# Performance work log

Hardware: AMD Instinct MI355X
Metric: run time of the kernel (lower is better)

The kernel has to match this reference:

```python
import jax, jax.numpy as jnp
import numpy as np

NUM_LAYERS = 2
D_MODEL = 64
D_INNER = 128   # expand * d_model
D_STATE = 128   # min(2*input_size, 256)
DT_RANK = 4     # ceil(d_model / 16)
D_CONV = 4
HIDDEN = 64


def _causal_dwconv(x, w, b):
    # x: [B, L, C], w: [C, K], b: [C]  -- causal depthwise conv (left pad K-1)
    K = w.shape[1]
    L = x.shape[1]
    xp = jnp.pad(x, ((0, 0), (K - 1, 0), (0, 0)))
    y = sum(xp[:, k:k + L, :] * w[:, k][None, None, :] for k in range(K))
    return y + b


def _selective_scan(u, delta, A, B, C, Dp):
    # u, delta: [b,L,d]; A: [d,n]; B, C: [b,L,n]; Dp: [d]
    dA = jnp.exp(jnp.einsum('bld,dn->lbdn', delta, A))          # [L,b,d,n]
    dBu = jnp.einsum('bld,bln,bld->lbdn', delta, B, u)           # [L,b,d,n]
    Ct = jnp.swapaxes(C, 0, 1)                                   # [L,b,n]

    def step(h, inp):
        dA_t, dBu_t, C_t = inp
        h = dA_t * h + dBu_t                                     # [b,d,n]
        y = jnp.einsum('bdn,bn->bd', h, C_t)
        return h, y

    h0 = jnp.zeros(dA.shape[1:], dA.dtype)
    _, ys = jax.lax.scan(step, h0, (dA, dBu, Ct))                # ys: [L,b,d]
    return jnp.swapaxes(ys, 0, 1) + u * Dp


def _mamba_layer(x, in_w, conv_w, conv_b, xproj_w, dt_w, dt_b, A_log, Dp, out_w):
    xz = x @ in_w.T                                              # [B,L,2*d_inner]
    xi, z = jnp.split(xz, 2, axis=-1)
    xi = jax.nn.silu(_causal_dwconv(xi, conv_w, conv_b))
    xdbl = xi @ xproj_w.T                                        # [B,L,dt_rank+2*d_state]
    delta = jax.nn.softplus(xdbl[..., :DT_RANK] @ dt_w.T + dt_b)
    Bm = xdbl[..., DT_RANK:DT_RANK + D_STATE]
    Cm = xdbl[..., DT_RANK + D_STATE:]
    A = -jnp.exp(A_log)
    y = _selective_scan(xi, delta, A, Bm, Cm, Dp)
    y = y * jax.nn.silu(z)
    return y @ out_w.T


def setup_inputs() -> dict:
    key = jax.random.key(0)
    ks = jax.random.split(key, 10)
    B, L = 4, 1024
    s = 0.05
    x = jax.random.normal(ks[0], (B, L, D_MODEL), dtype=jnp.float32)
    in_proj_w = jax.random.normal(ks[1], (NUM_LAYERS, 2 * D_INNER, D_MODEL)) * s
    conv_w = jax.random.normal(ks[2], (NUM_LAYERS, D_INNER, D_CONV)) * 0.2
    conv_b = jax.random.normal(ks[3], (NUM_LAYERS, D_INNER)) * 0.02
    x_proj_w = jax.random.normal(ks[4], (NUM_LAYERS, DT_RANK + 2 * D_STATE, D_INNER)) * s
    dt_w = jax.random.normal(ks[5], (NUM_LAYERS, D_INNER, DT_RANK)) * 0.1
    dt_b = jnp.full((NUM_LAYERS, D_INNER), -4.6, dtype=jnp.float32)  # softplus -> ~0.01
    # S4D-real init: A_log = log(1..d_state)
    A_log = jnp.log(jnp.broadcast_to(
        jnp.arange(1, D_STATE + 1, dtype=jnp.float32), (NUM_LAYERS, D_INNER, D_STATE)))
    D = jnp.ones((NUM_LAYERS, D_INNER), dtype=jnp.float32)
    out_proj_w = jax.random.normal(ks[6], (NUM_LAYERS, D_MODEL, D_INNER)) * s
    fc_w = jax.random.normal(ks[7], (HIDDEN, D_MODEL)) * s
    fc_b = jax.random.normal(ks[8], (HIDDEN,)) * 0.02
    return {"x": x, "in_proj_w": in_proj_w, "conv_w": conv_w, "conv_b": conv_b,
            "x_proj_w": x_proj_w, "dt_w": dt_w, "dt_b": dt_b, "A_log": A_log,
            "D": D, "out_proj_w": out_proj_w, "fc_w": fc_w, "fc_b": fc_b}


def reference(x, in_proj_w, conv_w, conv_b, x_proj_w, dt_w, dt_b, A_log, D, out_proj_w, fc_w, fc_b):
    h = x
    for l in range(NUM_LAYERS):
        h = _mamba_layer(h, in_proj_w[l], conv_w[l], conv_b[l], x_proj_w[l],
                         dt_w[l], dt_b[l], A_log[l], D[l], out_proj_w[l])
    return h @ fc_w.T + fc_b
```

## Files before the change

### kernel.cpp

```cpp
#include <hip/hip_runtime.h>
#include <hip/hip_bf16.h>

#define BB 4
#define LL 1024
#define DM 64
#define DI 128
#define DS 128
#define DTR 4
#define KC 4
#define RT 8
#define GRP 8
#define CS 64
#define NC 16
#define SCD 8
#define QL 32
#define L2E 1.44269504f

#define XWT_OFF   0
#define INWT_OFF  65536
#define OWT_OFF   98304
#define CWT_OFF   114688
#define CB_OFF    115712
#define DTWT_OFF  115968
#define DTB_OFF   116992
#define XWDT_OFF  117248

__device__ __forceinline__ float silu_f(float x) { return x / (1.f + __expf(-x)); }
__device__ __forceinline__ float ex2(float x) { return __builtin_amdgcn_exp2f(x); }

__device__ __forceinline__ float ldf(const void* p, long i, unsigned bf) {
    return bf ? __bfloat162float(((const __hip_bfloat16*)p)[i]) : ((const float*)p)[i];
}

__device__ __forceinline__ void fma4(float4& acc, float s, const float4 w) {
    acc.x = fmaf(s, w.x, acc.x); acc.y = fmaf(s, w.y, acc.y);
    acc.z = fmaf(s, w.z, acc.z); acc.w = fmaf(s, w.w, acc.w);
}

__device__ __forceinline__ void probe_flags(const void* dtb, const void* fcw,
                                            unsigned& bfe, unsigned& bfw) {
    unsigned w = *(const unsigned*)dtb;
    bfe = (w == 0xC093C093u) ? 1u : 0u;
    const unsigned* p = (const unsigned*)fcw;
    int cnt = 0;
    for (int i = 0; i < 32; ++i) {
        unsigned m = p[i] & 0x7FFFu;
        if (m >= 0x3000u && m < 0x4200u) cnt++;
    }
    bfw = (cnt >= 28) ? 1u : 0u;
}

__global__ __launch_bounds__(256) void k_prep(
        const void* __restrict__ inw, const void* __restrict__ xw,
        const void* __restrict__ ow, const void* __restrict__ cw,
        const void* __restrict__ cb, const void* __restrict__ dtw,
        const void* __restrict__ dtb, const void* __restrict__ fcw,
        unsigned* __restrict__ flags, float* __restrict__ WT) {
    unsigned bfe, bfw;
    probe_flags(dtb, fcw, bfe, bfw);
    int bid = blockIdx.x, tid = threadIdx.x;
    if (bid < 28) {
        const void* src; long soff; int srcK; float* dst; int dstN; int n0, k0;
        if (bid < 16) {
            int l = bid >> 3, kt = (bid >> 2) & 1, nt = bid & 3;
            src = xw; srcK = 128; soff = (long)l * 260 * 128 + 4 * 128;
            n0 = nt * 64; k0 = kt * 64; dst = WT + XWT_OFF + l * 32768; dstN = 256;
        } else if (bid < 24) {
            int b2 = bid - 16, l = b2 >> 2, nt = b2 & 3;
            src = inw; srcK = 64; soff = (long)l * 256 * 64;
            n0 = nt * 64; k0 = 0; dst = WT + INWT_OFF + l * 16384; dstN = 256;
        } else {
            int b2 = bid - 24, l = b2 >> 1, kt = b2 & 1;
            src = ow; srcK = 128; soff = (long)l * 64 * 128;
            n0 = 0; k0 = kt * 64; dst = WT + OWT_OFF + l * 8192; dstN = 64;
        }
        __shared__ float tile[64 * 65];
        for (int i = tid; i < 4096; i += 256) {
            int ln = i >> 6, lk = i & 63;
            tile[ln * 65 + lk] = ldf(src, soff + (long)(n0 + ln) * srcK + k0 + lk, bfw);
        }
        __syncthreads();
        for (int i = tid; i < 4096; i += 256) {
            int lk = i >> 6, ln = i & 63;
            dst[(long)(k0 + lk) * dstN + n0 + ln] = tile[ln * 65 + lk];
        }
    } else {
        if (tid == 0) { flags[0] = bfe; flags[1] = bfw; flags[2] = bfe & bfw; }
        for (int j = tid; j < 1024; j += 256) {
            int l = j >> 9, t = (j >> 7) & 3, d = j & 127;
            WT[CWT_OFF + j] = ldf(cw, (long)l * 512 + d * 4 + t, bfw);
        }
        for (int j = tid; j < 256; j += 256) WT[CB_OFF + j] = ldf(cb, j, bfw);
        for (int j = tid; j < 1024; j += 256) {
            int l = j >> 9, r = (j >> 7) & 3, d = j & 127;
            WT[DTWT_OFF + j] = ldf(dtw, (long)l * 512 + d * 4 + r, bfw);
        }
        for (int j = tid; j < 256; j += 256) WT[DTB_OFF + j] = ldf(dtb, j, bfe);
        for (int j = tid; j < 1024; j += 256) {
            int l = j >> 9, rem = j & 511;
            WT[XWDT_OFF + j] = ldf(xw, (long)l * 260 * 128 + rem, bfw);
        }
    }
}

__global__ __launch_bounds__(256) void k_inproj(
        const void* __restrict__ xin, int xin_probe,
        const float* __restrict__ wt, const unsigned* __restrict__ flags,
        float* __restrict__ xzx, float* __restrict__ sz) {
    unsigned bfx = xin_probe ? flags[0] : 0u;
    int row0 = blockIdx.x * RT;
    int tid = threadIdx.x, lane = tid & 63, g = tid >> 6;
    __shared__ float act[RT * DM];
    for (int i = tid; i < RT * DM; i += 256)
        act[i] = ldf(xin, (long)(row0 + (i >> 6)) * DM + (i & 63), bfx);
    __syncthreads();
    const float4* wt4 = (const float4*)wt;
    float4 acc[2];
    acc[0] = make_float4(0.f, 0.f, 0.f, 0.f);
    acc[1] = make_float4(0.f, 0.f, 0.f, 0.f);
#pragma unroll 8
    for (int k4 = 0; k4 < DM / 4; ++k4) {
        float4 w0 = wt4[(k4 * 4 + 0) * 64 + lane];
        float4 w1 = wt4[(k4 * 4 + 1) * 64 + lane];
        float4 w2 = wt4[(k4 * 4 + 2) * 64 + lane];
        float4 w3 = wt4[(k4 * 4 + 3) * 64 + lane];
#pragma unroll
        for (int r = 0; r < 2; ++r) {
            float4 av = *(const float4*)&act[(g * 2 + r) * DM + k4 * 4];
            fma4(acc[r], av.x, w0); fma4(acc[r], av.y, w1);
            fma4(acc[r], av.z, w2); fma4(acc[r], av.w, w3);
        }
    }
    int n0 = lane * 4;
#pragma unroll
    for (int r = 0; r < 2; ++r) {
        int row = row0 + g * 2 + r;
        if (n0 < DI) {
            *(float4*)&xzx[(size_t)row * DI + n0] = acc[r];
        } else {
            float4 v;
            v.x = silu_f(acc[r].x); v.y = silu_f(acc[r].y);
            v.z = silu_f(acc[r].z); v.w = silu_f(acc[r].w);
            *(float4*)&sz[(size_t)row * DI + (n0 - DI)] = v;
        }
    }
}

__global__ __launch_bounds__(256) void k_xproj(
        const float* __restrict__ xzx,
        const float* __restrict__ cwT, const float* __restrict__ cbF,
        const float* __restrict__ xwT, const float* __restrict__ xwdtF,
        const float* __restrict__ dtwT, const float* __restrict__ dtbF,
        float* __restrict__ xiw, float* __restrict__ dlt,
        float* __restrict__ Bm, float* __restrict__ Cm) {
    int row0 = blockIdx.x * RT;
    int b = row0 >> 10, l0 = row0 & (LL - 1);
    int tid = threadIdx.x, lane = tid & 63, g = tid >> 6;
    __shared__ float xc[(RT + KC - 1) * DI];
    __shared__ float act[RT * DI];
    __shared__ float dtp[RT * DTR];
    for (int i = tid; i < (RT + KC - 1) * DI; i += 256) {
        int r = (i >> 7) - (KC - 1);
        int l = l0 + r;
        xc[i] = (l >= 0) ? xzx[((size_t)b * LL + l) * DI + (i & 127)] : 0.f;
    }
    __syncthreads();
    for (int i = tid; i < RT * DI; i += 256) {
        int r = i >> 7, d = i & 127;
        float a = cbF[d];
#pragma unroll
        for (int t = 0; t < KC; ++t) a = fmaf(xc[(r + t) * DI + d], cwT[t * DI + d], a);
        float v = silu_f(a);
        act[i] = v;
        xiw[(size_t)(row0 + r) * DI + d] = v;
    }
    __syncthreads();
    const float4* wt4 = (const float4*)xwT;
    float4 acc[2];
    acc[0] = make_float4(0.f, 0.f, 0.f, 0.f);
    acc[1] = make_float4(0.f, 0.f, 0.f, 0.f);
#pragma unroll 8
    for (int k4 = 0; k4 < DI / 4; ++k4) {
        float4 w0 = wt4[(k4 * 4 + 0) * 64 + lane];
        float4 w1 = wt4[(k4 * 4 + 1) * 64 + lane];
        float4 w2 = wt4[(k4 * 4 + 2) * 64 + lane];
        float4 w3 = wt4[(k4 * 4 + 3) * 64 + lane];
#pragma unroll
        for (int r = 0; r < 2; ++r) {
            float4 av = *(const float4*)&act[(g * 2 + r) * DI + k4 * 4];
            fma4(acc[r], av.x, w0); fma4(acc[r], av.y, w1);
            fma4(acc[r], av.z, w2); fma4(acc[r], av.w, w3);
        }
    }
    int n0 = lane * 4;
#pragma unroll
    for (int r = 0; r < 2; ++r) {
        int row = row0 + g * 2 + r;
        if (n0 < DS) *(float4*)&Bm[(size_t)row * DS + n0] = acc[r];
        else         *(float4*)&Cm[(size_t)row * DS + (n0 - DS)] = acc[r];
    }
    if (tid < RT * DTR) {
        int r = tid >> 2, i = tid & 3;
        float a = 0.f;
#pragma unroll
        for (int k4 = 0; k4 < DI / 4; ++k4) {
            float4 av = *(const float4*)&act[r * DI + k4 * 4];
            float4 wv = *(const float4*)&xwdtF[i * DI + k4 * 4];
            a = fmaf(av.x, wv.x, a); a = fmaf(av.y, wv.y, a);
            a = fmaf(av.z, wv.z, a); a = fmaf(av.w, wv.w, a);
        }
        dtp[tid] = a;
    }
    __syncthreads();
    if (tid < DI) {
        float dw0 = dtwT[0 * DI + tid], dw1 = dtwT[1 * DI + tid];
        float dw2 = dtwT[2 * DI + tid], dw3 = dtwT[3 * DI + tid];
        float bv = dtbF[tid];
#pragma unroll
        for (int r = 0; r < RT; ++r) {
            float a = bv;
            a = fmaf(dtp[r * 4 + 0], dw0, a);
            a = fmaf(dtp[r * 4 + 1], dw1, a);
            a = fmaf(dtp[r * 4 + 2], dw2, a);
            a = fmaf(dtp[r * 4 + 3], dw3, a);
            dlt[(size_t)(row0 + r) * DI + tid] = (a > 20.f) ? a : log1pf(__expf(a));
        }
    }
}

__global__ __launch_bounds__(512) void k_scan1(
        const float* __restrict__ dlt, const float* __restrict__ xiw,
        const float* __restrict__ Bm, const float* __restrict__ Cm,
        const void* __restrict__ Alog, long aoff,
        const void* __restrict__ Dp, long doff,
        const unsigned* __restrict__ flags,
        float* __restrict__ hend, float* __restrict__ S,
        float* __restrict__ y) {
    __shared__ float Bsh[QL][DS];
    __shared__ float Csh[QL][DS];
    __shared__ float dsh[SCD][CS];
    __shared__ float dush[SCD][CS];
    __shared__ float ysh[CS][SCD];
    __shared__ float Wred[SCD * 520];
    int gid = blockIdx.x;
    int dg = gid / (BB * NC);
    int bc = gid % (BB * NC);
    int b = bc / NC, c = bc % NC;
    int d0 = dg * SCD;
    int tid = threadIdx.x, w = tid >> 6, t = tid & 63;
    int d = d0 + w, c0 = c * CS;
    unsigned bfe = flags[0];
    float A0 = -L2E * __expf(ldf(Alog, aoff + (long)d * DS + 2 * t, bfe));
    float A1 = -L2E * __expf(ldf(Alog, aoff + (long)d * DS + 2 * t + 1, bfe));
    {
        size_t src = ((size_t)b * LL + c0 + t) * DI + d0 + w;
        float dl = dlt[src], ul = xiw[src];
        dsh[w][t] = dl;
        dush[w][t] = dl * ul;
        ysh[t][w] = ul * ldf(Dp, doff + d0 + w, bfe);
    }
    float* Wl = Wred + w * 520;
    int rbase = (t >> 3) * 65 + (t & 7) * 8;
    float h0 = 0.f, h1v = 0.f, sumd = 0.f;
    for (int hh = 0; hh < 2; ++hh) {
        __syncthreads();
        for (int i = tid; i < QL * 32; i += 512) {
            int r = i >> 5, c4 = (i & 31) * 4;
            size_t g = ((size_t)b * LL + c0 + hh * QL + r) * DS + c4;
            *(float4*)&Bsh[r][c4] = *(const float4*)&Bm[g];
            *(float4*)&Csh[r][c4] = *(const float4*)&Cm[g];
        }
        __syncthreads();
        for (int li = 0; li < QL; li += GRP) {
            int lg = hh * QL + li;
            float dl[GRP], du[GRP], ea0[GRP], ea1[GRP], cv[GRP];
            float2 Bv[GRP], Cv[GRP];
#pragma unroll
            for (int s = 0; s < GRP; ++s) {
                dl[s] = dsh[w][lg + s];
                du[s] = dush[w][lg + s];
                Bv[s] = ((const float2*)Bsh[li + s])[t];
                Cv[s] = ((const float2*)Csh[li + s])[t];
            }
#pragma unroll
            for (int s = 0; s < GRP; ++s) {
                ea0[s] = ex2(dl[s] * A0);
                ea1[s] = ex2(dl[s] * A1);
                sumd += dl[s];
            }
#pragma unroll
            for (int s = 0; s < GRP; ++s) {
                h0  = fmaf(ea0[s], h0,  du[s] * Bv[s].x);
                h1v = fmaf(ea1[s], h1v, du[s] * Bv[s].y);
                cv[s] = fmaf(h0, Cv[s].x, h1v * Cv[s].y);
            }
#pragma unroll
            for (int s = 0; s < GRP; ++s) Wl[s * 65 + t] = cv[s];
            float pt = 0.f;
#pragma unroll
            for (int j = 0; j < 8; ++j) pt += Wl[rbase + j];
            pt += __shfl_xor(pt, 1, 64);
            pt += __shfl_xor(pt, 2, 64);
            pt += __shfl_xor(pt, 4, 64);
            if ((t & 7) == 0) ysh[lg + (t >> 3)][w] += pt;
        }
    }
    if (c < NC - 1) {
        size_t hbase = (((size_t)b * DI + d) * NC + c) * DS;
        ((float2*)(hend + hbase))[t] = make_float2(h0, h1v);
        if (t == 0) S[((size_t)b * DI + d) * NC + c] = sumd;
    }
    __syncthreads();
    for (int i = tid; i < CS * SCD; i += 512) {
        int l = i >> 3, dd = i & 7;
        y[((size_t)b * LL + c0 + l) * DI + d0 + dd] = ysh[l][dd];
    }
}

__global__ __launch_bounds__(512) void k_scan2(
        const float* __restrict__ dlt, const float* __restrict__ Cm,
        const void* __restrict__ Alog, long aoff,
        const unsigned* __restrict__ flags,
        const float* __restrict__ hend, const float* __restrict__ S,
        float* __restrict__ y) {
    __shared__ float Csh[QL][DS];
    __shared__ float cdsh[SCD][CS];
    __shared__ float ysh[CS][SCD];
    __shared__ float Wred[SCD * 520];
    int gid = blockIdx.x;
    int dg = gid / (BB * (NC - 1));
    int bc = gid % (BB * (NC - 1));
    int b = bc / (NC - 1), c = bc % (NC - 1) + 1;
    int d0 = dg * SCD;
    int tid = threadIdx.x, w = tid >> 6, t = tid & 63;
    int d = d0 + w, c0 = c * CS;
    unsigned bfe = flags[0];
    float A0 = -L2E * __expf(ldf(Alog, aoff + (long)d * DS + 2 * t, bfe));
    float A1 = -L2E * __expf(ldf(Alog, aoff + (long)d * DS + 2 * t + 1, bfe));
    {
        float a = dlt[((size_t)b * LL + c0 + t) * DI + d0 + w];
#pragma unroll
        for (int off = 1; off < 64; off <<= 1) {
            float nn = __shfl(a, t - off, 64);
            if (t >= off) a += nn;
        }
        cdsh[w][t] = a;
    }
    float hi0 = 0.f, hi1 = 0.f, ssum = 0.f;
    const float2* hep = (const float2*)(hend + (((size_t)b * DI + d) * NC) * DS);
    const float* Sp = S + ((size_t)b * DI + d) * NC;
    for (int cc = c - 1; cc >= 0; --cc) {
        float2 he = hep[(size_t)cc * (DS / 2) + t];
        hi0 = fmaf(ex2(A0 * ssum), he.x, hi0);
        hi1 = fmaf(ex2(A1 * ssum), he.y, hi1);
        ssum += Sp[cc];
    }
    float* Wl = Wred + w * 520;
    int rbase = (t >> 3) * 65 + (t & 7) * 8;
    for (int hh = 0; hh < 2; ++hh) {
        __syncthreads();
        for (int i = tid; i < QL * 32; i += 512) {
            int r = i >> 5, c4 = (i & 31) * 4;
            *(float4*)&Csh[r][c4] =
                *(const float4*)&Cm[((size_t)b * LL + c0 + hh * QL + r) * DS + c4];
        }
        __syncthreads();
        for (int li = 0; li < QL; li += GRP) {
            int lg = hh * QL + li;
            float cd[GRP], ea0[GRP], ea1[GRP], cv[GRP];
            float2 Cv[GRP];
#pragma unroll
            for (int s = 0; s < GRP; ++s) {
                cd[s] = cdsh[w][lg + s];
                Cv[s] = ((const float2*)Csh[li + s])[t];
            }
#pragma unroll
            for (int s = 0; s < GRP; ++s) {
                ea0[s] = ex2(cd[s] * A0);
                ea1[s] = ex2(cd[s] * A1);
            }
#pragma unroll
            for (int s = 0; s < GRP; ++s)
                cv[s] = fmaf(hi0 * ea0[s], Cv[s].x, hi1 * ea1[s] * Cv[s].y);
#pragma unroll
            for (int s = 0; s < GRP; ++s) Wl[s * 65 + t] = cv[s];
            float pt = 0.f;
#pragma unroll
            for (int j = 0; j < 8; ++j) pt += Wl[rbase + j];
            pt += __shfl_xor(pt, 1, 64);
            pt += __shfl_xor(pt, 2, 64);
            pt += __shfl_xor(pt, 4, 64);
            if ((t & 7) == 0) ysh[lg + (t >> 3)][w] = pt;
        }
    }
    __syncthreads();
    for (int i = tid; i < CS * SCD; i += 512) {
        int l = i >> 3, dd = i & 7;
        size_t idx = ((size_t)b * LL + c0 + l) * DI + d0 + dd;
        y[idx] += ysh[l][dd];
    }
}

__global__ __launch_bounds__(256) void k_out(
        const float* __restrict__ y, const float* __restrict__ sz,
        const float* __restrict__ owT, float* __restrict__ hout) {
    int row0 = blockIdx.x * RT;
    int tid = threadIdx.x, n = tid & 63, g = tid >> 6;
    __shared__ float act[RT * DI];
    for (int i = tid; i < RT * DI; i += 256) {
        size_t idx = (size_t)(row0 + (i >> 7)) * DI + (i & 127);
        act[i] = y[idx] * sz[idx];
    }
    __syncthreads();
    float acc[2] = {0.f, 0.f};
#pragma unroll 8
    for (int k4 = 0; k4 < DI / 4; ++k4) {
        float w0 = owT[(k4 * 4 + 0) * DM + n];
        float w1 = owT[(k4 * 4 + 1) * DM + n];
        float w2 = owT[(k4 * 4 + 2) * DM + n];
        float w3 = owT[(k4 * 4 + 3) * DM + n];
#pragma unroll
        for (int r = 0; r < 2; ++r) {
            float4 av = *(const float4*)&act[(g * 2 + r) * DI + k4 * 4];
            acc[r] = fmaf(av.x, w0, acc[r]); acc[r] = fmaf(av.y, w1, acc[r]);
            acc[r] = fmaf(av.z, w2, acc[r]); acc[r] = fmaf(av.w, w3, acc[r]);
        }
    }
#pragma unroll
    for (int r = 0; r < 2; ++r)
        hout[(size_t)(row0 + g * 2 + r) * DM + n] = acc[r];
}

__global__ __launch_bounds__(256) void k_fc(
        const float* __restrict__ h, const void* __restrict__ fw,
        const void* __restrict__ fb, const unsigned* __restrict__ flags,
        void* __restrict__ out) {
    unsigned bfw = flags[1], obf = flags[2];
    int row0 = blockIdx.x * RT;
    int tid = threadIdx.x, n = tid & 63, g = tid >> 6;
    __shared__ float wsh[DM * 65];
    __shared__ float act[RT * DM];
    for (int i = tid; i < DM * DM; i += 256) {
        int nn = i >> 6, k = i & 63;
        wsh[k * 65 + nn] = ldf(fw, i, bfw);
    }
    for (int i = tid; i < RT * DM; i += 256)
        act[i] = h[(size_t)(row0 + (i >> 6)) * DM + (i & 63)];
    __syncthreads();
    float bv = ldf(fb, n, bfw);
    float acc[2] = {bv, bv};
#pragma unroll 8
    for (int k4 = 0; k4 < DM / 4; ++k4) {
        float w0 = wsh[(k4 * 4 + 0) * 65 + n];
        float w1 = wsh[(k4 * 4 + 1) * 65 + n];
        float w2 = wsh[(k4 * 4 + 2) * 65 + n];
        float w3 = wsh[(k4 * 4 + 3) * 65 + n];
#pragma unroll
        for (int r = 0; r < 2; ++r) {
            float4 av = *(const float4*)&act[(g * 2 + r) * DM + k4 * 4];
            acc[r] = fmaf(av.x, w0, acc[r]); acc[r] = fmaf(av.y, w1, acc[r]);
            acc[r] = fmaf(av.z, w2, acc[r]); acc[r] = fmaf(av.w, w3, acc[r]);
        }
    }
#pragma unroll
    for (int r = 0; r < 2; ++r) {
        size_t idx = (size_t)(row0 + g * 2 + r) * DM + n;
        if (obf) ((__hip_bfloat16*)out)[idx] = __float2bfloat16(acc[r]);
        else     ((float*)out)[idx] = acc[r];
    }
}

extern "C" void kernel_launch(void* const* d_in, const int* in_sizes, int n_in,
                              void* d_out, int out_size, void* d_ws, size_t ws_size,
                              hipStream_t stream) {
    const void* x    = d_in[0];
    const void* inw  = d_in[1];
    const void* cw   = d_in[2];
    const void* cb   = d_in[3];
    const void* xw   = d_in[4];
    const void* dtw  = d_in[5];
    const void* dtb  = d_in[6];
    const void* Alog = d_in[7];
    const void* Dp   = d_in[8];
    const void* ow   = d_in[9];
    const void* fcw  = d_in[10];
    const void* fcb  = d_in[11];

    const size_t NBL = (size_t)BB * LL;
    const int GB = (int)(NBL / RT);
    unsigned* flags = (unsigned*)d_ws;
    float* base = (float*)d_ws + 64;
    float* h1   = base;
    float* sz   = h1 + 262144;
    float* xiw  = sz + 524288;
    float* dlt  = xiw + 524288;
    float* Bmw  = dlt + 524288;
    float* Cmw  = Bmw + 524288;
    float* yw   = Cmw + 524288;
    float* hend = yw + 524288;
    float* S    = hend + 1048576;
    float* xzx  = yw;
    float* WT   = (float*)d_out;

    k_prep<<<29, 256, 0, stream>>>(inw, xw, ow, cw, cb, dtw, dtb, fcw, flags, WT);

    for (int l = 0; l < 2; ++l) {
        const void* xin = (l == 0) ? x : (const void*)h1;
        int xmode = (l == 0) ? 1 : 0;
        k_inproj<<<GB, 256, 0, stream>>>(xin, xmode, WT + INWT_OFF + l * 16384, flags, xzx, sz);
        k_xproj<<<GB, 256, 0, stream>>>(xzx,
                                        WT + CWT_OFF + l * 512, WT + CB_OFF + l * 128,
                                        WT + XWT_OFF + l * 32768, WT + XWDT_OFF + l * 512,
                                        WT + DTWT_OFF + l * 512, WT + DTB_OFF + l * 128,
                                        xiw, dlt, Bmw, Cmw);
        long ao = (long)l * DI * DS;
        long dof = (long)l * DI;
        k_scan1<<<(DI / SCD) * BB * NC, 512, 0, stream>>>(
            dlt, xiw, Bmw, Cmw, Alog, ao, Dp, dof, flags, hend, S, yw);
        k_scan2<<<(DI / SCD) * BB * (NC - 1), 512, 0, stream>>>(
            dlt, Cmw, Alog, ao, flags, hend, S, yw);
        k_out<<<GB, 256, 0, stream>>>(yw, sz, WT + OWT_OFF + l * 8192, h1);
    }
    k_fc<<<GB, 256, 0, stream>>>(h1, fcw, fcb, flags, d_out);
}
```

Measured before the change: 292.1 us.

## Fuse all layer stages into one cooperative persistent kernel with grid syncs

Replaces the per-layer chain of eleven kernel launches with a single cooperative kernel. It loops over tiles for each stage and separates stages with grid-wide syncs, and the scan work is re-tiled to 4 channels per 256-thread block. The aim is to remove launch overhead and inter-kernel gaps. In exchange it adds the cost of grid barriers and threadfences, caps the grid at nb*256 blocks with nb at most 8, and the smaller scan tiles change how loads are reused.

Result: slower. 979.8 us (+235.4%).

```diff
diff --git a/kernel.cpp b/kernel.cpp
--- a/kernel.cpp
+++ b/kernel.cpp
@@ -1,5 +1,8 @@
 #include <hip/hip_runtime.h>
 #include <hip/hip_bf16.h>
+#include <hip/hip_cooperative_groups.h>
+
+namespace cg = cooperative_groups;
 
 #define BB 4
 #define LL 1024
@@ -12,8 +15,8 @@
 #define GRP 8
 #define CS 64
 #define NC 16
-#define SCD 8
-#define QL 32
+#define SCD 4
+#define QL 16
 #define L2E 1.44269504f
 
 #define XWT_OFF   0
@@ -103,6 +106,390 @@
     }
 }
 
+
+struct SM_s1 {
+    float Bsh[QL][DS];
+    float Csh[QL][DS];
+    float dsh[SCD][CS];
+    float dush[SCD][CS];
+    float ysh[CS][SCD];
+    float Wred[SCD * 520];
+};
+struct SM_s2 {
+    float Csh[QL][DS];
+    float cdsh[SCD][CS];
+    float ysh[CS][SCD];
+    float Wred[SCD * 520];
+};
+struct SM_ip { float act[RT * DM]; };
+struct SM_xp { float xc[(RT + KC - 1) * DI]; float act[RT * DI]; float dtp[RT * DTR]; };
+struct SM_o  { float act[RT * DI]; };
+struct SM_f  { float wsh[DM * 65]; float act[RT * DM]; };
+union SMem {
+    SM_s1 s1; SM_s2 s2; SM_ip ip; SM_xp xp; SM_o o; SM_f f;
+};
+
+__global__ __launch_bounds__(256) void k_mega(
+        const void* __restrict__ x, const float* __restrict__ WT,
+        const unsigned* __restrict__ flags,
+        float* __restrict__ h1, float* __restrict__ sz,
+        float* __restrict__ xiw, float* __restrict__ dlt,
+        float* __restrict__ Bm, float* __restrict__ Cm,
+        float* __restrict__ y, float* __restrict__ hend, float* __restrict__ S,
+        const void* __restrict__ Alog, const void* __restrict__ Dp,
+        const void* __restrict__ fcw, const void* __restrict__ fcb,
+        void* __restrict__ out) {
+    cg::grid_group grid = cg::this_grid();
+    __shared__ SMem sm;
+    int tid = threadIdx.x;
+    int lane = tid & 63, g4 = tid >> 6;
+    unsigned bfe = flags[0], bfw = flags[1], obf = flags[2];
+    float* xzx = y;
+
+    for (int l = 0; l < 2; ++l) {
+        const float* inwT  = WT + INWT_OFF + l * 16384;
+        const float* xwT   = WT + XWT_OFF + l * 32768;
+        const float* cwT   = WT + CWT_OFF + l * 512;
+        const float* cbF   = WT + CB_OFF + l * 128;
+        const float* dtwT  = WT + DTWT_OFF + l * 512;
+        const float* dtbF  = WT + DTB_OFF + l * 128;
+        const float* xwdtF = WT + XWDT_OFF + l * 512;
+        const float* owT   = WT + OWT_OFF + l * 8192;
+        long aoff = (long)l * DI * DS;
+        long doff = (long)l * DI;
+        const void* xin = (l == 0) ? x : (const void*)h1;
+        unsigned bfx = (l == 0) ? bfe : 0u;
+
+        for (int tile = blockIdx.x; tile < 512; tile += gridDim.x) {
+            __syncthreads();
+            int row0 = tile * RT;
+            for (int i = tid; i < RT * DM; i += 256)
+                sm.ip.act[i] = ldf(xin, (long)(row0 + (i >> 6)) * DM + (i & 63), bfx);
+            __syncthreads();
+            const float4* wt4 = (const float4*)inwT;
+            float4 acc[2];
+            acc[0] = make_float4(0.f, 0.f, 0.f, 0.f);
+            acc[1] = make_float4(0.f, 0.f, 0.f, 0.f);
+#pragma unroll 8
+            for (int k4 = 0; k4 < DM / 4; ++k4) {
+                float4 w0 = wt4[(k4 * 4 + 0) * 64 + lane];
+                float4 w1 = wt4[(k4 * 4 + 1) * 64 + lane];
+                float4 w2 = wt4[(k4 * 4 + 2) * 64 + lane];
+                float4 w3 = wt4[(k4 * 4 + 3) * 64 + lane];
+#pragma unroll
+                for (int r = 0; r < 2; ++r) {
+                    float4 av = *(const float4*)&sm.ip.act[(g4 * 2 + r) * DM + k4 * 4];
+                    fma4(acc[r], av.x, w0); fma4(acc[r], av.y, w1);
+                    fma4(acc[r], av.z, w2); fma4(acc[r], av.w, w3);
+                }
+            }
+            int n0 = lane * 4;
+#pragma unroll
+            for (int r = 0; r < 2; ++r) {
+                int row = row0 + g4 * 2 + r;
+                if (n0 < DI) {
+                    *(float4*)&xzx[(size_t)row * DI + n0] = acc[r];
+                } else {
+                    float4 v;
+                    v.x = silu_f(acc[r].x); v.y = silu_f(acc[r].y);
+                    v.z = silu_f(acc[r].z); v.w = silu_f(acc[r].w);
+                    *(float4*)&sz[(size_t)row * DI + (n0 - DI)] = v;
+                }
+            }
+        }
+        __threadfence(); grid.sync();
+
+        for (int tile = blockIdx.x; tile < 512; tile += gridDim.x) {
+            __syncthreads();
+            int row0 = tile * RT;
+            int b = row0 >> 10, l0 = row0 & (LL - 1);
+            for (int i = tid; i < (RT + KC - 1) * DI; i += 256) {
+                int r = (i >> 7) - (KC - 1);
+                int ll2 = l0 + r;
+                sm.xp.xc[i] = (ll2 >= 0) ? xzx[((size_t)b * LL + ll2) * DI + (i & 127)] : 0.f;
+            }
+            __syncthreads();
+            for (int i = tid; i < RT * DI; i += 256) {
+                int r = i >> 7, d = i & 127;
+                float a = cbF[d];
+#pragma unroll
+                for (int t = 0; t < KC; ++t)
+                    a = fmaf(sm.xp.xc[(r + t) * DI + d], cwT[t * DI + d], a);
+                float v = silu_f(a);
+                sm.xp.act[i] = v;
+                xiw[(size_t)(row0 + r) * DI + d] = v;
+            }
+            __syncthreads();
+            const float4* wt4 = (const float4*)xwT;
+            float4 acc[2];
+            acc[0] = make_float4(0.f, 0.f, 0.f, 0.f);
+            acc[1] = make_float4(0.f, 0.f, 0.f, 0.f);
+#pragma unroll 8
+            for (int k4 = 0; k4 < DI / 4; ++k4) {
+                float4 w0 = wt4[(k4 * 4 + 0) * 64 + lane];
+                float4 w1 = wt4[(k4 * 4 + 1) * 64 + lane];
+                float4 w2 = wt4[(k4 * 4 + 2) * 64 + lane];
+                float4 w3 = wt4[(k4 * 4 + 3) * 64 + lane];
+#pragma unroll
+                for (int r = 0; r < 2; ++r) {
+                    float4 av = *(const float4*)&sm.xp.act[(g4 * 2 + r) * DI + k4 * 4];
+                    fma4(acc[r], av.x, w0); fma4(acc[r], av.y, w1);
+                    fma4(acc[r], av.z, w2); fma4(acc[r], av.w, w3);
+                }
+            }
+            int n0 = lane * 4;
+#pragma unroll
+            for (int r = 0; r < 2; ++r) {
+                int row = row0 + g4 * 2 + r;
+                if (n0 < DS) *(float4*)&Bm[(size_t)row * DS + n0] = acc[r];
+                else         *(float4*)&Cm[(size_t)row * DS + (n0 - DS)] = acc[r];
+            }
+            if (tid < RT * DTR) {
+                int r = tid >> 2, i = tid & 3;
+                float a = 0.f;
+#pragma unroll
+                for (int k4 = 0; k4 < DI / 4; ++k4) {
+                    float4 av = *(const float4*)&sm.xp.act[r * DI + k4 * 4];
+                    float4 wv = *(const float4*)&xwdtF[i * DI + k4 * 4];
+                    a = fmaf(av.x, wv.x, a); a = fmaf(av.y, wv.y, a);
+                    a = fmaf(av.z, wv.z, a); a = fmaf(av.w, wv.w, a);
+                }
+                sm.xp.dtp[tid] = a;
+            }
+            __syncthreads();
+            if (tid < DI) {
+                float dw0 = dtwT[0 * DI + tid], dw1 = dtwT[1 * DI + tid];
+                float dw2 = dtwT[2 * DI + tid], dw3 = dtwT[3 * DI + tid];
+                float bv = dtbF[tid];
+#pragma unroll
+                for (int r = 0; r < RT; ++r) {
+                    float a = bv;
+                    a = fmaf(sm.xp.dtp[r * 4 + 0], dw0, a);
+                    a = fmaf(sm.xp.dtp[r * 4 + 1], dw1, a);
+                    a = fmaf(sm.xp.dtp[r * 4 + 2], dw2, a);
+                    a = fmaf(sm.xp.dtp[r * 4 + 3], dw3, a);
+                    dlt[(size_t)(row0 + r) * DI + tid] = (a > 20.f) ? a : log1pf(__expf(a));
+                }
+            }
+        }
+        __threadfence(); grid.sync();
+
+        for (int u = blockIdx.x; u < (DI / SCD) * BB * NC; u += gridDim.x) {
+            __syncthreads();
+            int dg = u >> 6;
+            int bc = u & 63;
+            int b = bc >> 4, c = bc & 15;
+            int d0 = dg * SCD;
+            int w = g4, t = lane;
+            int d = d0 + w, c0 = c * CS;
+            float A0 = -L2E * __expf(ldf(Alog, aoff + (long)d * DS + 2 * t, bfe));
+            float A1 = -L2E * __expf(ldf(Alog, aoff + (long)d * DS + 2 * t + 1, bfe));
+            {
+                size_t src = ((size_t)b * LL + c0 + t) * DI + d0 + w;
+                float dl = dlt[src], ul = xiw[src];
+                sm.s1.dsh[w][t] = dl;
+                sm.s1.dush[w][t] = dl * ul;
+                sm.s1.ysh[t][w] = ul * ldf(Dp, doff + d0 + w, bfe);
+            }
+            float* Wl = sm.s1.Wred + w * 520;
+            int rbase = (t >> 3) * 65 + (t & 7) * 8;
+            float h0 = 0.f, h1v = 0.f, sumd = 0.f;
+            for (int qq = 0; qq < CS / QL; ++qq) {
+                __syncthreads();
+                for (int i = tid; i < QL * 32; i += 256) {
+                    int r = i >> 5, c4 = (i & 31) * 4;
+                    size_t gsrc = ((size_t)b * LL + c0 + qq * QL + r) * DS + c4;
+                    *(float4*)&sm.s1.Bsh[r][c4] = *(const float4*)&Bm[gsrc];
+                    *(float4*)&sm.s1.Csh[r][c4] = *(const float4*)&Cm[gsrc];
+                }
+                __syncthreads();
+                for (int li = 0; li < QL; li += GRP) {
+                    int lg = qq * QL + li;
+                    float dl[GRP], du[GRP], ea0[GRP], ea1[GRP], cv[GRP];
+                    float2 Bv[GRP], Cv[GRP];
+#pragma unroll
+                    for (int s = 0; s < GRP; ++s) {
+                        dl[s] = sm.s1.dsh[w][lg + s];
+                        du[s] = sm.s1.dush[w][lg + s];
+                        Bv[s] = ((const float2*)sm.s1.Bsh[li + s])[t];
+                        Cv[s] = ((const float2*)sm.s1.Csh[li + s])[t];
+                    }
+#pragma unroll
+                    for (int s = 0; s < GRP; ++s) {
+                        ea0[s] = ex2(dl[s] * A0);
+                        ea1[s] = ex2(dl[s] * A1);
+                        sumd += dl[s];
+                    }
+#pragma unroll
+                    for (int s = 0; s < GRP; ++s) {
+                        h0  = fmaf(ea0[s], h0,  du[s] * Bv[s].x);
+                        h1v = fmaf(ea1[s], h1v, du[s] * Bv[s].y);
+                        cv[s] = fmaf(h0, Cv[s].x, h1v * Cv[s].y);
+                    }
+#pragma unroll
+                    for (int s = 0; s < GRP; ++s) Wl[s * 65 + t] = cv[s];
+                    float pt = 0.f;
+#pragma unroll
+                    for (int j = 0; j < 8; ++j) pt += Wl[rbase + j];
+                    pt += __shfl_xor(pt, 1, 64);
+                    pt += __shfl_xor(pt, 2, 64);
+                    pt += __shfl_xor(pt, 4, 64);
+                    if ((t & 7) == 0) sm.s1.ysh[lg + (t >> 3)][w] += pt;
+                }
+            }
+            if (c < NC - 1) {
+                size_t hbase = (((size_t)b * DI + d) * NC + c) * DS;
+                ((float2*)(hend + hbase))[t] = make_float2(h0, h1v);
+                if (t == 0) S[((size_t)b * DI + d) * NC + c] = sumd;
+            }
+            __syncthreads();
+            for (int i = tid; i < CS * SCD; i += 256) {
+                int ll2 = i >> 2, dd = i & 3;
+                y[((size_t)b * LL + c0 + ll2) * DI + d0 + dd] = sm.s1.ysh[ll2][dd];
+            }
+        }
+        __threadfence(); grid.sync();
+
+        for (int u = blockIdx.x; u < (DI / SCD) * BB * (NC - 1); u += gridDim.x) {
+            __syncthreads();
+            int dg = u / (BB * (NC - 1));
+            int bc = u % (BB * (NC - 1));
+            int b = bc / (NC - 1), c = bc % (NC - 1) + 1;
+            int d0 = dg * SCD;
+            int w = g4, t = lane;
+            int d = d0 + w, c0 = c * CS;
+            float A0 = -L2E * __expf(ldf(Alog, aoff + (long)d * DS + 2 * t, bfe));
+            float A1 = -L2E * __expf(ldf(Alog, aoff + (long)d * DS + 2 * t + 1, bfe));
+            {
+                float a = dlt[((size_t)b * LL + c0 + t) * DI + d0 + w];
+#pragma unroll
+                for (int off = 1; off < 64; off <<= 1) {
+                    float nn = __shfl(a, t - off, 64);
+                    if (t >= off) a += nn;
+                }
+                sm.s2.cdsh[w][t] = a;
+            }
+            float hi0 = 0.f, hi1 = 0.f, ssum = 0.f;
+            const float2* hep = (const float2*)(hend + (((size_t)b * DI + d) * NC) * DS);
+            const float* Sp = S + ((size_t)b * DI + d) * NC;
+            for (int cc = c - 1; cc >= 0; --cc) {
+                float2 he = hep[(size_t)cc * (DS / 2) + t];
+                hi0 = fmaf(ex2(A0 * ssum), he.x, hi0);
+                hi1 = fmaf(ex2(A1 * ssum), he.y, hi1);
+                ssum += Sp[cc];
+            }
+            float* Wl = sm.s2.Wred + w * 520;
+            int rbase = (t >> 3) * 65 + (t & 7) * 8;
+            for (int qq = 0; qq < CS / QL; ++qq) {
+                __syncthreads();
+                for (int i = tid; i < QL * 32; i += 256) {
+                    int r = i >> 5, c4 = (i & 31) * 4;
+                    *(float4*)&sm.s2.Csh[r][c4] =
+                        *(const float4*)&Cm[((size_t)b * LL + c0 + qq * QL + r) * DS + c4];
+                }
+                __syncthreads();
+                for (int li = 0; li < QL; li += GRP) {
+                    int lg = qq * QL + li;
+                    float cd[GRP], ea0[GRP], ea1[GRP], cv[GRP];
+                    float2 Cv[GRP];
+#pragma unroll
+                    for (int s = 0; s < GRP; ++s) {
+                        cd[s] = sm.s2.cdsh[w][lg + s];
+                        Cv[s] = ((const float2*)sm.s2.Csh[li + s])[t];
+                    }
+#pragma unroll
+                    for (int s = 0; s < GRP; ++s) {
+                        ea0[s] = ex2(cd[s] * A0);
+                        ea1[s] = ex2(cd[s] * A1);
+                    }
+#pragma unroll
+                    for (int s = 0; s < GRP; ++s)
+                        cv[s] = fmaf(hi0 * ea0[s], Cv[s].x, hi1 * ea1[s] * Cv[s].y);
+#pragma unroll
+                    for (int s = 0; s < GRP; ++s) Wl[s * 65 + t] = cv[s];
+                    float pt = 0.f;
+#pragma unroll
+                    for (int j = 0; j < 8; ++j) pt += Wl[rbase + j];
+                    pt += __shfl_xor(pt, 1, 64);
+                    pt += __shfl_xor(pt, 2, 64);
+                    pt += __shfl_xor(pt, 4, 64);
+                    if ((t & 7) == 0) sm.s2.ysh[lg + (t >> 3)][w] = pt;
+                }
+            }
+            __syncthreads();
+            for (int i = tid; i < CS * SCD; i += 256) {
+                int ll2 = i >> 2, dd = i & 3;
+                size_t idx = ((size_t)b * LL + c0 + ll2) * DI + d0 + dd;
+                y[idx] += sm.s2.ysh[ll2][dd];
+            }
+        }
+        __threadfence(); grid.sync();
+
+        for (int tile = blockIdx.x; tile < 512; tile += gridDim.x) {
+            __syncthreads();
+            int row0 = tile * RT;
+            int n = lane;
+            for (int i = tid; i < RT * DI; i += 256) {
+                size_t idx = (size_t)(row0 + (i >> 7)) * DI + (i & 127);
+                sm.o.act[i] = y[idx] * sz[idx];
+            }
+            __syncthreads();
+            float acc[2] = {0.f, 0.f};
+#pragma unroll 8
+            for (int k4 = 0; k4 < DI / 4; ++k4) {
+                float w0 = owT[(k4 * 4 + 0) * DM + n];
+                float w1 = owT[(k4 * 4 + 1) * DM + n];
+                float w2 = owT[(k4 * 4 + 2) * DM + n];
+                float w3 = owT[(k4 * 4 + 3) * DM + n];
+#pragma unroll
+                for (int r = 0; r < 2; ++r) {
+                    float4 av = *(const float4*)&sm.o.act[(g4 * 2 + r) * DI + k4 * 4];
+                    acc[r] = fmaf(av.x, w0, acc[r]); acc[r] = fmaf(av.y, w1, acc[r]);
+                    acc[r] = fmaf(av.z, w2, acc[r]); acc[r] = fmaf(av.w, w3, acc[r]);
+                }
+            }
+#pragma unroll
+            for (int r = 0; r < 2; ++r)
+                h1[(size_t)(row0 + g4 * 2 + r) * DM + n] = acc[r];
+        }
+        __threadfence(); grid.sync();
+    }
+
+    for (int tile = blockIdx.x; tile < 512; tile += gridDim.x) {
+        __syncthreads();
+        int row0 = tile * RT;
+        int n = lane;
+        for (int i = tid; i < DM * DM; i += 256) {
+            int nn = i >> 6, k = i & 63;
+            sm.f.wsh[k * 65 + nn] = ldf(fcw, i, bfw);
+        }
+        for (int i = tid; i < RT * DM; i += 256)
+            sm.f.act[i] = h1[(size_t)(row0 + (i >> 6)) * DM + (i & 63)];
+        __syncthreads();
+        float bv = ldf(fcb, n, bfw);
+        float acc[2] = {bv, bv};
+#pragma unroll 8
+        for (int k4 = 0; k4 < DM / 4; ++k4) {
+            float w0 = sm.f.wsh[(k4 * 4 + 0) * 65 + n];
+            float w1 = sm.f.wsh[(k4 * 4 + 1) * 65 + n];
+            float w2 = sm.f.wsh[(k4 * 4 + 2) * 65 + n];
+            float w3 = sm.f.wsh[(k4 * 4 + 3) * 65 + n];
+#pragma unroll
+            for (int r = 0; r < 2; ++r) {
+                float4 av = *(const float4*)&sm.f.act[(g4 * 2 + r) * DM + k4 * 4];
+                acc[r] = fmaf(av.x, w0, acc[r]); acc[r] = fmaf(av.y, w1, acc[r]);
+                acc[r] = fmaf(av.z, w2, acc[r]); acc[r] = fmaf(av.w, w3, acc[r]);
+            }
+        }
+#pragma unroll
+        for (int r = 0; r < 2; ++r) {
+            size_t idx = (size_t)(row0 + g4 * 2 + r) * DM + n;
+            if (obf) ((__hip_bfloat16*)out)[idx] = __float2bfloat16(acc[r]);
+            else     ((float*)out)[idx] = acc[r];
+        }
+    }
+}
+
 __global__ __launch_bounds__(256) void k_inproj(
         const void* __restrict__ xin, int xin_probe,
         const float* __restrict__ wt, const unsigned* __restrict__ flags,
@@ -228,6 +615,7 @@
     }
 }
 
+#define FQL 32
 __global__ __launch_bounds__(512) void k_scan1(
         const float* __restrict__ dlt, const float* __restrict__ xiw,
         const float* __restrict__ Bm, const float* __restrict__ Cm,
@@ -236,17 +624,17 @@
         const unsigned* __restrict__ flags,
         float* __restrict__ hend, float* __restrict__ S,
         float* __restrict__ y) {
-    __shared__ float Bsh[QL][DS];
-    __shared__ float Csh[QL][DS];
-    __shared__ float dsh[SCD][CS];
-    __shared__ float dush[SCD][CS];
-    __shared__ float ysh[CS][SCD];
-    __shared__ float Wred[SCD * 520];
+    __shared__ float Bsh[FQL][DS];
+    __shared__ float Csh[FQL][DS];
+    __shared__ float dsh[8][CS];
+    __shared__ float dush[8][CS];
+    __shared__ float ysh[CS][8];
+    __shared__ float Wred[8 * 520];
     int gid = blockIdx.x;
     int dg = gid / (BB * NC);
     int bc = gid % (BB * NC);
     int b = bc / NC, c = bc % NC;
-    int d0 = dg * SCD;
+    int d0 = dg * 8;
     int tid = threadIdx.x, w = tid >> 6, t = tid & 63;
     int d = d0 + w, c0 = c * CS;
     unsigned bfe = flags[0];
@@ -264,15 +652,15 @@
     float h0 = 0.f, h1v = 0.f, sumd = 0.f;
     for (int hh = 0; hh < 2; ++hh) {
         __syncthreads();
-        for (int i = tid; i < QL * 32; i += 512) {
+        for (int i = tid; i < FQL * 32; i += 512) {
             int r = i >> 5, c4 = (i & 31) * 4;
-            size_t g = ((size_t)b * LL + c0 + hh * QL + r) * DS + c4;
+            size_t g = ((size_t)b * LL + c0 + hh * FQL + r) * DS + c4;
             *(float4*)&Bsh[r][c4] = *(const float4*)&Bm[g];
             *(float4*)&Csh[r][c4] = *(const float4*)&Cm[g];
         }
         __syncthreads();
-        for (int li = 0; li < QL; li += GRP) {
-            int lg = hh * QL + li;
+        for (int li = 0; li < FQL; li += GRP) {
+            int lg = hh * FQL + li;
             float dl[GRP], du[GRP], ea0[GRP], ea1[GRP], cv[GRP];
             float2 Bv[GRP], Cv[GRP];
 #pragma unroll
@@ -311,7 +699,7 @@
         if (t == 0) S[((size_t)b * DI + d) * NC + c] = sumd;
     }
     __syncthreads();
-    for (int i = tid; i < CS * SCD; i += 512) {
+    for (int i = tid; i < CS * 8; i += 512) {
         int l = i >> 3, dd = i & 7;
         y[((size_t)b * LL + c0 + l) * DI + d0 + dd] = ysh[l][dd];
     }
@@ -323,15 +711,15 @@
         const unsigned* __restrict__ flags,
         const float* __restrict__ hend, const float* __restrict__ S,
         float* __restrict__ y) {
-    __shared__ float Csh[QL][DS];
-    __shared__ float cdsh[SCD][CS];
-    __shared__ float ysh[CS][SCD];
-    __shared__ float Wred[SCD * 520];
+    __shared__ float Csh[FQL][DS];
+    __shared__ float cdsh[8][CS];
+    __shared__ float ysh[CS][8];
+    __shared__ float Wred[8 * 520];
     int gid = blockIdx.x;
     int dg = gid / (BB * (NC - 1));
     int bc = gid % (BB * (NC - 1));
     int b = bc / (NC - 1), c = bc % (NC - 1) + 1;
-    int d0 = dg * SCD;
+    int d0 = dg * 8;
     int tid = threadIdx.x, w = tid >> 6, t = tid & 63;
     int d = d0 + w, c0 = c * CS;
     unsigned bfe = flags[0];
@@ -359,14 +747,14 @@
     int rbase = (t >> 3) * 65 + (t & 7) * 8;
     for (int hh = 0; hh < 2; ++hh) {
         __syncthreads();
-        for (int i = tid; i < QL * 32; i += 512) {
+        for (int i = tid; i < FQL * 32; i += 512) {
             int r = i >> 5, c4 = (i & 31) * 4;
             *(float4*)&Csh[r][c4] =
-                *(const float4*)&Cm[((size_t)b * LL + c0 + hh * QL + r) * DS + c4];
+                *(const float4*)&Cm[((size_t)b * LL + c0 + hh * FQL + r) * DS + c4];
         }
         __syncthreads();
-        for (int li = 0; li < QL; li += GRP) {
-            int lg = hh * QL + li;
+        for (int li = 0; li < FQL; li += GRP) {
+            int lg = hh * FQL + li;
             float cd[GRP], ea0[GRP], ea1[GRP], cv[GRP];
             float2 Cv[GRP];
 #pragma unroll
@@ -394,7 +782,7 @@
         }
     }
     __syncthreads();
-    for (int i = tid; i < CS * SCD; i += 512) {
+    for (int i = tid; i < CS * 8; i += 512) {
         int l = i >> 3, dd = i & 7;
         size_t idx = ((size_t)b * LL + c0 + l) * DI + d0 + dd;
         y[idx] += ysh[l][dd];
@@ -504,22 +892,37 @@
 
     k_prep<<<29, 256, 0, stream>>>(inw, xw, ow, cw, cb, dtw, dtb, fcw, flags, WT);
 
-    for (int l = 0; l < 2; ++l) {
-        const void* xin = (l == 0) ? x : (const void*)h1;
-        int xmode = (l == 0) ? 1 : 0;
-        k_inproj<<<GB, 256, 0, stream>>>(xin, xmode, WT + INWT_OFF + l * 16384, flags, xzx, sz);
-        k_xproj<<<GB, 256, 0, stream>>>(xzx,
-                                        WT + CWT_OFF + l * 512, WT + CB_OFF + l * 128,
-                                        WT + XWT_OFF + l * 32768, WT + XWDT_OFF + l * 512,
-                                        WT + DTWT_OFF + l * 512, WT + DTB_OFF + l * 128,
-                                        xiw, dlt, Bmw, Cmw);
-        long ao = (long)l * DI * DS;
-        long dof = (long)l * DI;
-        k_scan1<<<(DI / SCD) * BB * NC, 512, 0, stream>>>(
-            dlt, xiw, Bmw, Cmw, Alog, ao, Dp, dof, flags, hend, S, yw);
-        k_scan2<<<(DI / SCD) * BB * (NC - 1), 512, 0, stream>>>(
-            dlt, Cmw, Alog, ao, flags, hend, S, yw);
-        k_out<<<GB, 256, 0, stream>>>(yw, sz, WT + OWT_OFF + l * 8192, h1);
-    }
-    k_fc<<<GB, 256, 0, stream>>>(h1, fcw, fcb, flags, d_out);
-}
+    int nb = 0;
+    hipOccupancyMaxActiveBlocksPerMultiprocessor(&nb, k_mega, 256, 0);
+    if (nb >= 1) {
+        if (nb > 8) nb = 8;
+        const float* WT_c = WT; const unsigned* fl_c = flags;
+        void* params[] = {
+            (void*)&x, (void*)&WT_c, (void*)&fl_c,
+            (void*)&h1, (void*)&sz, (void*)&xiw, (void*)&dlt,
+            (void*)&Bmw, (void*)&Cmw, (void*)&yw, (void*)&hend, (void*)&S,
+            (void*)&Alog, (void*)&Dp, (void*)&fcw, (void*)&fcb, (void*)&d_out
+        };
+        hipLaunchCooperativeKernel((const void*)k_mega, dim3(nb * 256),
+                                   dim3(256), params, 0, stream);
+    } else {
+        for (int l = 0; l < 2; ++l) {
+            const void* xin = (l == 0) ? x : (const void*)h1;
+            int xmode = (l == 0) ? 1 : 0;
+            k_inproj<<<GB, 256, 0, stream>>>(xin, xmode, WT + INWT_OFF + l * 16384, flags, xzx, sz);
+            k_xproj<<<GB, 256, 0, stream>>>(xzx,
+                                            WT + CWT_OFF + l * 512, WT + CB_OFF + l * 128,
+                                            WT + XWT_OFF + l * 32768, WT + XWDT_OFF + l * 512,
+                                            WT + DTWT_OFF + l * 512, WT + DTB_OFF + l * 128,
+                                            xiw, dlt, Bmw, Cmw);
+            long ao = (long)l * DI * DS;
+            long dof = (long)l * DI;
+            k_scan1<<<16 * BB * NC, 512, 0, stream>>>(
+                dlt, xiw, Bmw, Cmw, Alog, ao, Dp, dof, flags, hend, S, yw);
+            k_scan2<<<16 * BB * (NC - 1), 512, 0, stream>>>(
+                dlt, Cmw, Alog, ao, flags, hend, S, yw);
+            k_out<<<GB, 256, 0, stream>>>(yw, sz, WT + OWT_OFF + l * 8192, h1);
+        }
+        k_fc<<<GB, 256, 0, stream>>>(h1, fcw, fcb, flags, d_out);
+    }
+}
```
